# Optimization experiments

Measured on AMD Instinct MI355X. Metric: run time of the kernel, lower is better.

Reference implementation:

```python
import jax, jax.numpy as jnp
from jax import lax
import numpy as np

B, C, H, W = 16, 1, 1024, 1024


def _erode(x, ksize=3):
    # torch: zero-pad then min over ksize x ksize window
    pad = (ksize - 1) // 2
    xp = jnp.pad(x, ((0, 0), (0, 0), (pad, pad), (pad, pad)))  # constant 0, matches F.pad
    return lax.reduce_window(xp, jnp.array(jnp.inf, x.dtype), lax.min,
                             (1, 1, ksize, ksize), (1, 1, 1, 1), 'VALID')


def _circle_weights(y_true):
    e1 = _erode(y_true)
    e2 = _erode(e1)
    e3 = _erode(e2)
    e4 = _erode(e3)
    circle_all = (0.4 * (y_true - e1) + 0.5 * (e1 - e2)
                  + 0.6 * (e2 - e3) + 0.7 * (e3 - e4))
    circle_all = jnp.where(circle_all == 0, jnp.asarray(0.8, circle_all.dtype), circle_all)
    return lax.stop_gradient(circle_all)  # computed under torch.no_grad()


def setup_inputs() -> dict:
    key = jax.random.key(0)
    k1, k2 = jax.random.split(key)
    y_pred = jax.random.uniform(k1, (B, C, H, W), dtype=jnp.float32)
    # binary-ish segmentation mask so erosion rings are non-trivial
    y_true = (jax.random.uniform(k2, (B, C, H, W)) > 0.7).astype(jnp.float32)
    return {"y_pred": y_pred, "y_true": y_true}


def reference(y_pred, y_true):
    w = _circle_weights(y_true)
    loss = (y_pred - y_true) ** 2 * w  # MSELoss(reduction='none') * weights
    return (loss.mean(axis=(1, 2, 3)), loss.mean())
```

## Files before the change

kernel.cpp:

```cpp
#include <hip/hip_runtime.h>
#include <stdint.h>

#define BATCH 16
#define HH 1024
#define WW 1024
#define TH 8
#define HALO 4
#define ROWS (TH + 2*HALO)
#define WORDS (WW/64)
#define NTHREADS 256
#define NWAVES (NTHREADS/64)

__global__ __launch_bounds__(NTHREADS) void circle_mse_kernel(
    const float* __restrict__ y_pred,
    const float* __restrict__ y_true,
    float* __restrict__ out)
{
    __shared__ unsigned long long bits0[ROWS][WORDS];
    __shared__ unsigned long long cur[ROWS][WORDS];
    __shared__ unsigned long long tmp[ROWS][WORDS];
    __shared__ unsigned long long E[4][TH][WORDS];
    __shared__ float wavesum[NWAVES];

    const int tid  = threadIdx.x;
    const int lane = tid & 63;
    const int wave = tid >> 6;

    const int im = blockIdx.x / (HH / TH);
    const int rb = blockIdx.x % (HH / TH);
    const int r0 = rb * TH - HALO;

    const float* yt = y_true + (size_t)im * HH * WW;
    const float* yp = y_pred + (size_t)im * HH * WW;

    #pragma unroll 8
    for (int p = wave; p < ROWS * WORDS; p += NWAVES) {
        int row  = p >> 4;
        int word = p & (WORDS - 1);
        int gr   = r0 + row;
        unsigned long long m = 0ull;
        if (gr >= 0 && gr < HH) {
            float v = yt[(size_t)gr * WW + word * 64 + lane];
            m = __ballot(v != 0.0f);
        }
        if (lane == 0) { bits0[row][word] = m; cur[row][word] = m; }
    }
    __syncthreads();

    for (int k = 1; k <= 4; ++k) {
        int lo = k - 1, hi = ROWS - (k - 1);
        for (int p = tid; p < (hi - lo) * WORDS; p += NTHREADS) {
            int row  = lo + (p >> 4);
            int word = p & (WORDS - 1);
            unsigned long long m = cur[row][word];
            unsigned long long l = (word > 0)         ? cur[row][word - 1] : 0ull;
            unsigned long long r = (word < WORDS - 1) ? cur[row][word + 1] : 0ull;
            tmp[row][word] = m & ((m << 1) | (l >> 63)) & ((m >> 1) | (r << 63));
        }
        __syncthreads();
        lo = k; hi = ROWS - k;
        for (int p = tid; p < (hi - lo) * WORDS; p += NTHREADS) {
            int row  = lo + (p >> 4);
            int word = p & (WORDS - 1);
            unsigned long long res = tmp[row - 1][word] & tmp[row][word] & tmp[row + 1][word];
            cur[row][word] = res;
            if (row >= HALO && row < HALO + TH) E[k - 1][row - HALO][word] = res;
        }
        __syncthreads();
    }

    const int word = tid >> 4;
    const int bsh  = (tid & 15) * 4;
    float lsum = 0.0f;
    #pragma unroll
    for (int row = 0; row < TH; ++row) {
        int gr = r0 + HALO + row;
        float4 pv = *reinterpret_cast<const float4*>(&yp[(size_t)gr * WW + tid * 4]);
        unsigned int y4 = (unsigned int)((bits0[row + HALO][word] >> bsh) & 0xFull);
        unsigned int n1 = (unsigned int)((E[0][row][word] >> bsh) & 0xFull);
        unsigned int n2 = (unsigned int)((E[1][row][word] >> bsh) & 0xFull);
        unsigned int n3 = (unsigned int)((E[2][row][word] >> bsh) & 0xFull);
        unsigned int n4 = (unsigned int)((E[3][row][word] >> bsh) & 0xFull);
        float pvals[4] = {pv.x, pv.y, pv.z, pv.w};
        #pragma unroll
        for (int j = 0; j < 4; ++j) {
            unsigned int y = (y4 >> j) & 1u;
            unsigned int c = y + ((n1 >> j) & 1u) + ((n2 >> j) & 1u)
                               + ((n3 >> j) & 1u) + ((n4 >> j) & 1u);
            float w = (c == 0u || c == 5u) ? 0.8f : (0.3f + 0.1f * (float)c);
            float d = pvals[j] - (float)y;
            lsum += d * d * w;
        }
    }

    for (int off = 32; off > 0; off >>= 1)
        lsum += __shfl_down(lsum, off, 64);
    if (lane == 0) wavesum[wave] = lsum;
    __syncthreads();
    if (tid == 0) {
        float s = 0.0f;
        for (int wv = 0; wv < NWAVES; ++wv) s += wavesum[wv];
        atomicAdd(&out[im], s * (1.0f / (float)(HH * WW)));
        atomicAdd(&out[BATCH], s * (1.0f / ((float)BATCH * (float)(HH * WW))));
    }
}

extern "C" void kernel_launch(void* const* d_in, const int* in_sizes, int n_in,
                              void* d_out, int out_size, void* d_ws, size_t ws_size,
                              hipStream_t stream) {
    const float* y_pred = (const float*)d_in[0];
    const float* y_true = (const float*)d_in[1];
    float* out = (float*)d_out;

    hipMemsetAsync(d_out, 0, (size_t)out_size * sizeof(float), stream);

    dim3 grid(BATCH * (HH / TH));
    circle_mse_kernel<<<grid, NTHREADS, 0, stream>>>(y_pred, y_true, out);
}
```

Measured before the change: 181.8 us.

## Pre-pack y_true into a global bitmask before fused erosion and MSE

Adds a separate pack kernel that turns y_true into a 64-bit-per-word bitmask in workspace, so the main kernel reads packed bits instead of re-reading float halo rows. This removes the redundant halo float loads, which were 16 rows per 8 output rows. The erosion steps are also fused into one pass per iteration using ping-pong buffers, which halves the barriers. In exchange it adds a second kernel launch and a global round trip for the bitmask, and it falls back to the old kernel when no workspace is available.

```diff
diff --git a/kernel.cpp b/kernel.cpp
--- a/kernel.cpp
+++ b/kernel.cpp
@@ -10,15 +10,32 @@
 #define WORDS (WW/64)
 #define NTHREADS 256
 #define NWAVES (NTHREADS/64)
-
-__global__ __launch_bounds__(NTHREADS) void circle_mse_kernel(
+#define TOTAL_WORDS (BATCH * HH * WORDS)
+
+__global__ __launch_bounds__(NTHREADS) void pack_kernel(
+    const float* __restrict__ y_true,
+    unsigned long long* __restrict__ packed)
+{
+    const int lane = threadIdx.x & 63;
+    const size_t base = ((size_t)((blockIdx.x * NTHREADS + threadIdx.x) >> 6)) * 64;
+    unsigned long long mine = 0ull;
+    #pragma unroll 16
+    for (int i = 0; i < 64; ++i) {
+        float v = y_true[(base + (size_t)i) * 64 + lane];
+        unsigned long long m = __ballot(v != 0.0f);
+        mine = (lane == i) ? m : mine;
+    }
+    packed[base + lane] = mine;
+}
+
+__global__ __launch_bounds__(NTHREADS) void erode_mse_kernel(
     const float* __restrict__ y_pred,
-    const float* __restrict__ y_true,
+    const unsigned long long* __restrict__ packed,
     float* __restrict__ out)
 {
     __shared__ unsigned long long bits0[ROWS][WORDS];
-    __shared__ unsigned long long cur[ROWS][WORDS];
-    __shared__ unsigned long long tmp[ROWS][WORDS];
+    __shared__ unsigned long long bufA[ROWS][WORDS];
+    __shared__ unsigned long long bufB[ROWS][WORDS];
     __shared__ unsigned long long E[4][TH][WORDS];
     __shared__ float wavesum[NWAVES];
 
@@ -30,40 +47,50 @@
     const int rb = blockIdx.x % (HH / TH);
     const int r0 = rb * TH - HALO;
 
-    const float* yt = y_true + (size_t)im * HH * WW;
     const float* yp = y_pred + (size_t)im * HH * WW;
 
-    #pragma unroll 8
-    for (int p = wave; p < ROWS * WORDS; p += NWAVES) {
-        int row  = p >> 4;
-        int word = p & (WORDS - 1);
+    {
+        int row  = tid >> 4;
+        int word = tid & (WORDS - 1);
         int gr   = r0 + row;
         unsigned long long m = 0ull;
-        if (gr >= 0 && gr < HH) {
-            float v = yt[(size_t)gr * WW + word * 64 + lane];
-            m = __ballot(v != 0.0f);
-        }
-        if (lane == 0) { bits0[row][word] = m; cur[row][word] = m; }
-    }
-    __syncthreads();
-
+        if (gr >= 0 && gr < HH)
+            m = packed[((size_t)im * HH + gr) * WORDS + word];
+        bits0[row][word] = m;
+        bufA[row][word]  = m;
+    }
+    __syncthreads();
+
+    #pragma unroll
     for (int k = 1; k <= 4; ++k) {
-        int lo = k - 1, hi = ROWS - (k - 1);
-        for (int p = tid; p < (hi - lo) * WORDS; p += NTHREADS) {
-            int row  = lo + (p >> 4);
-            int word = p & (WORDS - 1);
-            unsigned long long m = cur[row][word];
-            unsigned long long l = (word > 0)         ? cur[row][word - 1] : 0ull;
-            unsigned long long r = (word < WORDS - 1) ? cur[row][word + 1] : 0ull;
-            tmp[row][word] = m & ((m << 1) | (l >> 63)) & ((m >> 1) | (r << 63));
-        }
-        __syncthreads();
-        lo = k; hi = ROWS - k;
-        for (int p = tid; p < (hi - lo) * WORDS; p += NTHREADS) {
-            int row  = lo + (p >> 4);
-            int word = p & (WORDS - 1);
-            unsigned long long res = tmp[row - 1][word] & tmp[row][word] & tmp[row + 1][word];
-            cur[row][word] = res;
+        unsigned long long (*src)[WORDS] = (k & 1) ? bufA : bufB;
+        unsigned long long (*dst)[WORDS] = (k & 1) ? bufB : bufA;
+        int lo = k, hi = ROWS - k;
+        int n  = (hi - lo) * WORDS;
+        if (tid < n) {
+            int row  = lo + (tid >> 4);
+            int word = tid & (WORDS - 1);
+            unsigned long long h0, h1, h2;
+            {
+                unsigned long long m = src[row - 1][word];
+                unsigned long long l = (word > 0)         ? src[row - 1][word - 1] : 0ull;
+                unsigned long long r = (word < WORDS - 1) ? src[row - 1][word + 1] : 0ull;
+                h0 = m & ((m << 1) | (l >> 63)) & ((m >> 1) | (r << 63));
+            }
+            {
+                unsigned long long m = src[row][word];
+                unsigned long long l = (word > 0)         ? src[row][word - 1] : 0ull;
+                unsigned long long r = (word < WORDS - 1) ? src[row][word + 1] : 0ull;
+                h1 = m & ((m << 1) | (l >> 63)) & ((m >> 1) | (r << 63));
+            }
+            {
+                unsigned long long m = src[row + 1][word];
+                unsigned long long l = (word > 0)         ? src[row + 1][word - 1] : 0ull;
+                unsigned long long r = (word < WORDS - 1) ? src[row + 1][word + 1] : 0ull;
+                h2 = m & ((m << 1) | (l >> 63)) & ((m >> 1) | (r << 63));
+            }
+            unsigned long long res = h0 & h1 & h2;
+            dst[row][word] = res;
             if (row >= HALO && row < HALO + TH) E[k - 1][row - HALO][word] = res;
         }
         __syncthreads();
@@ -105,6 +132,97 @@
     }
 }
 
+__global__ __launch_bounds__(NTHREADS) void circle_mse_kernel(
+    const float* __restrict__ y_pred,
+    const float* __restrict__ y_true,
+    float* __restrict__ out)
+{
+    __shared__ unsigned long long bits0[ROWS][WORDS];
+    __shared__ unsigned long long cur[ROWS][WORDS];
+    __shared__ unsigned long long tmp[ROWS][WORDS];
+    __shared__ unsigned long long E[4][TH][WORDS];
+    __shared__ float wavesum[NWAVES];
+
+    const int tid  = threadIdx.x;
+    const int lane = tid & 63;
+    const int wave = tid >> 6;
+    const int im = blockIdx.x / (HH / TH);
+    const int rb = blockIdx.x % (HH / TH);
+    const int r0 = rb * TH - HALO;
+    const float* yt = y_true + (size_t)im * HH * WW;
+    const float* yp = y_pred + (size_t)im * HH * WW;
+
+    #pragma unroll 8
+    for (int p = wave; p < ROWS * WORDS; p += NWAVES) {
+        int row  = p >> 4;
+        int word = p & (WORDS - 1);
+        int gr   = r0 + row;
+        unsigned long long m = 0ull;
+        if (gr >= 0 && gr < HH) {
+            float v = yt[(size_t)gr * WW + word * 64 + lane];
+            m = __ballot(v != 0.0f);
+        }
+        if (lane == 0) { bits0[row][word] = m; cur[row][word] = m; }
+    }
+    __syncthreads();
+
+    for (int k = 1; k <= 4; ++k) {
+        int lo = k - 1, hi = ROWS - (k - 1);
+        for (int p = tid; p < (hi - lo) * WORDS; p += NTHREADS) {
+            int row  = lo + (p >> 4);
+            int word = p & (WORDS - 1);
+            unsigned long long m = cur[row][word];
+            unsigned long long l = (word > 0)         ? cur[row][word - 1] : 0ull;
+            unsigned long long r = (word < WORDS - 1) ? cur[row][word + 1] : 0ull;
+            tmp[row][word] = m & ((m << 1) | (l >> 63)) & ((m >> 1) | (r << 63));
+        }
+        __syncthreads();
+        lo = k; hi = ROWS - k;
+        for (int p = tid; p < (hi - lo) * WORDS; p += NTHREADS) {
+            int row  = lo + (p >> 4);
+            int word = p & (WORDS - 1);
+            unsigned long long res = tmp[row - 1][word] & tmp[row][word] & tmp[row + 1][word];
+            cur[row][word] = res;
+            if (row >= HALO && row < HALO + TH) E[k - 1][row - HALO][word] = res;
+        }
+        __syncthreads();
+    }
+
+    const int word = tid >> 4;
+    const int bsh  = (tid & 15) * 4;
+    float lsum = 0.0f;
+    #pragma unroll
+    for (int row = 0; row < TH; ++row) {
+        int gr = r0 + HALO + row;
+        float4 pv = *reinterpret_cast<const float4*>(&yp[(size_t)gr * WW + tid * 4]);
+        unsigned int y4 = (unsigned int)((bits0[row + HALO][word] >> bsh) & 0xFull);
+        unsigned int n1 = (unsigned int)((E[0][row][word] >> bsh) & 0xFull);
+        unsigned int n2 = (unsigned int)((E[1][row][word] >> bsh) & 0xFull);
+        unsigned int n3 = (unsigned int)((E[2][row][word] >> bsh) & 0xFull);
+        unsigned int n4 = (unsigned int)((E[3][row][word] >> bsh) & 0xFull);
+        float pvals[4] = {pv.x, pv.y, pv.z, pv.w};
+        #pragma unroll
+        for (int j = 0; j < 4; ++j) {
+            unsigned int y = (y4 >> j) & 1u;
+            unsigned int c = y + ((n1 >> j) & 1u) + ((n2 >> j) & 1u)
+                               + ((n3 >> j) & 1u) + ((n4 >> j) & 1u);
+            float w = (c == 0u || c == 5u) ? 0.8f : (0.3f + 0.1f * (float)c);
+            float d = pvals[j] - (float)y;
+            lsum += d * d * w;
+        }
+    }
+    for (int off = 32; off > 0; off >>= 1)
+        lsum += __shfl_down(lsum, off, 64);
+    if (lane == 0) wavesum[wave] = lsum;
+    __syncthreads();
+    if (tid == 0) {
+        float s = 0.0f;
+        for (int wv = 0; wv < NWAVES; ++wv) s += wavesum[wv];
+        atomicAdd(&out[im], s * (1.0f / (float)(HH * WW)));
+        atomicAdd(&out[BATCH], s * (1.0f / ((float)BATCH * (float)(HH * WW))));
+    }
+}
+
 extern "C" void kernel_launch(void* const* d_in, const int* in_sizes, int n_in,
                               void* d_out, int out_size, void* d_ws, size_t ws_size,
                               hipStream_t stream) {
@@ -114,6 +232,12 @@
 
     hipMemsetAsync(d_out, 0, (size_t)out_size * sizeof(float), stream);
 
-    dim3 grid(BATCH * (HH / TH));
-    circle_mse_kernel<<<grid, NTHREADS, 0, stream>>>(y_pred, y_true, out);
-}
+    const size_t need = (size_t)TOTAL_WORDS * sizeof(unsigned long long);
+    if (ws_size >= need && d_ws != nullptr) {
+        unsigned long long* packed = (unsigned long long*)d_ws;
+        pack_kernel<<<dim3(TOTAL_WORDS / 64 / NWAVES), NTHREADS, 0, stream>>>(y_true, packed);
+        erode_mse_kernel<<<dim3(BATCH * (HH / TH)), NTHREADS, 0, stream>>>(y_pred, packed, out);
+    } else {
+        circle_mse_kernel<<<dim3(BATCH * (HH / TH)), NTHREADS, 0, stream>>>(y_pred, y_true, out);
+    }
+}
```

After: 169.1 us. 1.08x faster.

## Split into pack, per-row register erosion, and deterministic reduce kernels

Applied to the files above, without the earlier changes.

Adds a pre-pass that bit-packs y_true into the workspace so each image row is read once as floats. A per-row kernel then loads a 9-row packed window into shared memory and performs all four erosions in registers on a 12-bit neighbourhood per thread, which removes the halo recomputation and the repeated barriers of the tiled version. Per-row partial sums go to the workspace and a single-block kernel reduces them, replacing atomics and the memset. The cost is two extra launches and a workspace round-trip; the old kernel remains as a fallback, with padded shared arrays.

```diff
diff --git a/kernel.cpp b/kernel.cpp
--- a/kernel.cpp
+++ b/kernel.cpp
@@ -4,32 +4,178 @@
 #define BATCH 16
 #define HH 1024
 #define WW 1024
+#define WORDS (WW/64)
+#define NTHREADS 256
+#define NWAVES (NTHREADS/64)
+#define TOTAL_WORDS (BATCH * HH * WORDS)
+#define NBLOCKS_WIN (BATCH * HH)
+#define PACK_BLOCKS (TOTAL_WORDS / 32 / NWAVES)
+
+typedef unsigned long long u64;
+
+__global__ __launch_bounds__(NTHREADS) void pack_kernel(
+    const float* __restrict__ y_true,
+    u64* __restrict__ packed)
+{
+    const int lane = threadIdx.x & 63;
+    const size_t base = ((size_t)((blockIdx.x * NTHREADS + threadIdx.x) >> 6)) * 32;
+    u64 mine = 0ull;
+    #pragma unroll
+    for (int i = 0; i < 32; ++i) {
+        float v = y_true[(base + (size_t)i) * 64 + lane];
+        u64 m = __ballot(v != 0.0f);
+        mine = (lane == i) ? m : mine;
+    }
+    if (lane < 32) packed[base + lane] = mine;
+}
+
+__global__ __launch_bounds__(NTHREADS) void erode_mse_win_kernel(
+    const float* __restrict__ y_pred,
+    const u64* __restrict__ packed,
+    float* __restrict__ ws_partial)
+{
+    __shared__ u64 rows_s[9][WORDS];
+    __shared__ float wavesum[NWAVES];
+
+    const int tid = threadIdx.x;
+    const int lane = tid & 63;
+    const int wave = tid >> 6;
+    const int b  = blockIdx.x;
+    const int im = b >> 10;
+    const int r  = b & (HH - 1);
+
+    const size_t pidx = ((size_t)im * HH + r) * (WW / 4) + tid;
+    float4 p = reinterpret_cast<const float4*>(y_pred)[pidx];
+
+    if (tid < 9 * WORDS) {
+        int d = tid >> 4, w = tid & (WORDS - 1);
+        int rr = r - 4 + d;
+        rows_s[d][w] = (rr >= 0 && rr < HH)
+                     ? packed[((size_t)im * HH + rr) * WORDS + w] : 0ull;
+    }
+    __syncthreads();
+
+    const int w  = tid >> 4;
+    const int sh = ((tid & 15) << 2) - 4;
+    unsigned int win[9];
+    #pragma unroll
+    for (int d = 0; d < 9; ++d) {
+        u64 C = rows_s[d][w];
+        u64 L = (w > 0)         ? rows_s[d][w - 1] : 0ull;
+        u64 R = (w < WORDS - 1) ? rows_s[d][w + 1] : 0ull;
+        u64 t;
+        if (sh >= 0) {
+            t = C >> sh;
+            if (sh > 52) t |= R << (64 - sh);
+        } else {
+            t = (C << 4) | (L >> 60);
+        }
+        win[d] = (unsigned int)t & 0xFFFu;
+    }
+
+    int c0 = (win[4] >> 4) & 1, c1 = (win[4] >> 5) & 1,
+        c2 = (win[4] >> 6) & 1, c3 = (win[4] >> 7) & 1;
+
+    unsigned int h[9];
+    #pragma unroll
+    for (int d = 0; d < 9; ++d) h[d] = win[d] & (win[d] << 1) & (win[d] >> 1);
+    #pragma unroll
+    for (int d = 1; d < 8; ++d) win[d] = h[d - 1] & h[d] & h[d + 1];
+    c0 += (win[4] >> 4) & 1; c1 += (win[4] >> 5) & 1;
+    c2 += (win[4] >> 6) & 1; c3 += (win[4] >> 7) & 1;
+    #pragma unroll
+    for (int d = 1; d < 8; ++d) h[d] = win[d] & (win[d] << 1) & (win[d] >> 1);
+    #pragma unroll
+    for (int d = 2; d < 7; ++d) win[d] = h[d - 1] & h[d] & h[d + 1];
+    c0 += (win[4] >> 4) & 1; c1 += (win[4] >> 5) & 1;
+    c2 += (win[4] >> 6) & 1; c3 += (win[4] >> 7) & 1;
+    #pragma unroll
+    for (int d = 2; d < 7; ++d) h[d] = win[d] & (win[d] << 1) & (win[d] >> 1);
+    #pragma unroll
+    for (int d = 3; d < 6; ++d) win[d] = h[d - 1] & h[d] & h[d + 1];
+    c0 += (win[4] >> 4) & 1; c1 += (win[4] >> 5) & 1;
+    c2 += (win[4] >> 6) & 1; c3 += (win[4] >> 7) & 1;
+    #pragma unroll
+    for (int d = 3; d < 6; ++d) h[d] = win[d] & (win[d] << 1) & (win[d] >> 1);
+    win[4] = h[3] & h[4] & h[5];
+    c0 += (win[4] >> 4) & 1; c1 += (win[4] >> 5) & 1;
+    c2 += (win[4] >> 6) & 1; c3 += (win[4] >> 7) & 1;
+
+    float pv[4] = {p.x, p.y, p.z, p.w};
+    int   cc[4] = {c0, c1, c2, c3};
+    float lsum = 0.0f;
+    #pragma unroll
+    for (int j = 0; j < 4; ++j) {
+        int   c = cc[j];
+        float y = (c != 0) ? 1.0f : 0.0f;
+        float wt = (c == 0 || c == 5) ? 0.8f : (0.3f + 0.1f * (float)c);
+        float d = pv[j] - y;
+        lsum += d * d * wt;
+    }
+
+    for (int off = 32; off > 0; off >>= 1)
+        lsum += __shfl_down(lsum, off, 64);
+    if (lane == 0) wavesum[wave] = lsum;
+    __syncthreads();
+    if (tid == 0) {
+        float s = 0.0f;
+        for (int wv = 0; wv < NWAVES; ++wv) s += wavesum[wv];
+        ws_partial[b] = s;
+    }
+}
+
+__global__ __launch_bounds__(NTHREADS) void reduce_kernel(
+    const float* __restrict__ partial,
+    float* __restrict__ out)
+{
+    __shared__ float ssum[NTHREADS];
+    __shared__ float imsum[BATCH];
+    const int tid = threadIdx.x;
+    const int im    = tid >> 4;
+    const int chunk = tid & 15;
+    size_t base = (size_t)im * (HH) + (size_t)chunk * 64;
+    float s = 0.0f;
+    #pragma unroll 8
+    for (int j = 0; j < 64; ++j) s += partial[base + j];
+    ssum[tid] = s;
+    __syncthreads();
+    if (tid < BATCH) {
+        float a = 0.0f;
+        #pragma unroll
+        for (int t = 0; t < 16; ++t) a += ssum[tid * 16 + t];
+        imsum[tid] = a;
+        out[tid] = a * (1.0f / (float)(HH * WW));
+    }
+    __syncthreads();
+    if (tid == 0) {
+        float tot = 0.0f;
+        #pragma unroll
+        for (int i = 0; i < BATCH; ++i) tot += imsum[i];
+        out[BATCH] = tot * (1.0f / ((float)BATCH * (float)(HH * WW)));
+    }
+}
+
 #define TH 8
 #define HALO 4
 #define ROWS (TH + 2*HALO)
-#define WORDS (WW/64)
-#define NTHREADS 256
-#define NWAVES (NTHREADS/64)
-
+#define WPAD (WORDS + 1)
 __global__ __launch_bounds__(NTHREADS) void circle_mse_kernel(
     const float* __restrict__ y_pred,
     const float* __restrict__ y_true,
     float* __restrict__ out)
 {
-    __shared__ unsigned long long bits0[ROWS][WORDS];
-    __shared__ unsigned long long cur[ROWS][WORDS];
-    __shared__ unsigned long long tmp[ROWS][WORDS];
-    __shared__ unsigned long long E[4][TH][WORDS];
+    __shared__ u64 bits0[ROWS][WPAD];
+    __shared__ u64 cur[ROWS][WPAD];
+    __shared__ u64 tmp[ROWS][WPAD];
+    __shared__ u64 E[4][TH][WPAD];
     __shared__ float wavesum[NWAVES];
 
     const int tid  = threadIdx.x;
     const int lane = tid & 63;
     const int wave = tid >> 6;
-
     const int im = blockIdx.x / (HH / TH);
     const int rb = blockIdx.x % (HH / TH);
     const int r0 = rb * TH - HALO;
-
     const float* yt = y_true + (size_t)im * HH * WW;
     const float* yp = y_pred + (size_t)im * HH * WW;
 
@@ -38,7 +184,7 @@
         int row  = p >> 4;
         int word = p & (WORDS - 1);
         int gr   = r0 + row;
-        unsigned long long m = 0ull;
+        u64 m = 0ull;
         if (gr >= 0 && gr < HH) {
             float v = yt[(size_t)gr * WW + word * 64 + lane];
             m = __ballot(v != 0.0f);
@@ -52,9 +198,9 @@
         for (int p = tid; p < (hi - lo) * WORDS; p += NTHREADS) {
             int row  = lo + (p >> 4);
             int word = p & (WORDS - 1);
-            unsigned long long m = cur[row][word];
-            unsigned long long l = (word > 0)         ? cur[row][word - 1] : 0ull;
-            unsigned long long r = (word < WORDS - 1) ? cur[row][word + 1] : 0ull;
+            u64 m = cur[row][word];
+            u64 l = (word > 0)         ? cur[row][word - 1] : 0ull;
+            u64 r = (word < WORDS - 1) ? cur[row][word + 1] : 0ull;
             tmp[row][word] = m & ((m << 1) | (l >> 63)) & ((m >> 1) | (r << 63));
         }
         __syncthreads();
@@ -62,7 +208,7 @@
         for (int p = tid; p < (hi - lo) * WORDS; p += NTHREADS) {
             int row  = lo + (p >> 4);
             int word = p & (WORDS - 1);
-            unsigned long long res = tmp[row - 1][word] & tmp[row][word] & tmp[row + 1][word];
+            u64 res = tmp[row - 1][word] & tmp[row][word] & tmp[row + 1][word];
             cur[row][word] = res;
             if (row >= HALO && row < HALO + TH) E[k - 1][row - HALO][word] = res;
         }
@@ -92,7 +238,6 @@
             lsum += d * d * w;
         }
     }
-
     for (int off = 32; off > 0; off >>= 1)
         lsum += __shfl_down(lsum, off, 64);
     if (lane == 0) wavesum[wave] = lsum;
@@ -112,8 +257,17 @@
     const float* y_true = (const float*)d_in[1];
     float* out = (float*)d_out;
 
-    hipMemsetAsync(d_out, 0, (size_t)out_size * sizeof(float), stream);
-
-    dim3 grid(BATCH * (HH / TH));
-    circle_mse_kernel<<<grid, NTHREADS, 0, stream>>>(y_pred, y_true, out);
-}
+    const size_t need = (size_t)TOTAL_WORDS * sizeof(u64)
+                      + (size_t)NBLOCKS_WIN * sizeof(float);
+    if (ws_size >= need && d_ws != nullptr) {
+        u64* packed = (u64*)d_ws;
+        float* ws_partial = (float*)(packed + TOTAL_WORDS);
+        pack_kernel<<<dim3(PACK_BLOCKS), NTHREADS, 0, stream>>>(y_true, packed);
+        erode_mse_win_kernel<<<dim3(NBLOCKS_WIN), NTHREADS, 0, stream>>>(
+            y_pred, packed, ws_partial);
+        reduce_kernel<<<dim3(1), NTHREADS, 0, stream>>>(ws_partial, out);
+    } else {
+        hipMemsetAsync(d_out, 0, (size_t)out_size * sizeof(float), stream);
+        circle_mse_kernel<<<dim3(BATCH * (HH / TH)), NTHREADS, 0, stream>>>(y_pred, y_true, out);
+    }
+}
```

New measurement: 159.6 us. -12.2%, faster.
